# Kernel optimization log

Hardware: AMD Instinct MI355X
Metric: run time of the kernel (lower is better)

The kernel has to match this reference:

```python
import jax, jax.numpy as jnp
import numpy as np

K_SIZE = 5
PAD = 2  # (dilation*(k-1)+1 - stride + 1)//2 with k=5, dilation=1, stride=1
DEPTH_MAX = 192.0
SAMPLE_NUM = 15


def setup_inputs() -> dict:
    key = jax.random.key(0)
    k1, k2, k3, k4 = jax.random.split(key, 4)
    b, c, h, w = 2, 32, 256, 512
    depth = jax.random.uniform(k1, (b, 1, h, w), jnp.float32) * 100.0
    features = jax.random.normal(k2, (b, c, h, w), jnp.float32)
    guide_weight = jax.random.uniform(k3, (b, h, w, K_SIZE * K_SIZE), jnp.float32)
    sample_idx = jax.random.randint(k4, (SAMPLE_NUM,), 0, K_SIZE * K_SIZE, dtype=jnp.int32)
    return {"depth": depth, "features": features, "guide_weight": guide_weight,
            "sample_idx": sample_idx}


def _gather(xpad, rows, cols):
    # xpad [b,c,H+2p,W+2p]; rows [s,h], cols [s,w] -> [b,c,s,h,w]
    return xpad[:, :, rows[:, :, None], cols[:, None, :]]


def reference(depth, features, guide_weight, sample_idx):
    b, c, h, w = features.shape
    d = depth.reshape(b, h, w)
    valid = ((d > 0) & (d < DEPTH_MAX)).astype(features.dtype)[:, None]  # [b,1,h,w]

    # Gaussian positional weights of the sampled kernel offsets (select_index)
    ctr = K_SIZE // 2
    px = (sample_idx % K_SIZE).astype(jnp.float32)
    py = (sample_idx // K_SIZE).astype(jnp.float32)
    dis = jnp.sqrt((px - ctr) ** 2 + (py - ctr) ** 2)
    pos_w = jnp.exp(-0.5 * dis)
    pos_w = pos_w / jnp.sum(pos_w)  # [s]

    # Direct gather at sampled kernel offsets (equivalent to unfold + index_select).
    # torch Unfold kernel-position ordering is row-major: p -> (ky=p//K, kx=p%K).
    dy = sample_idx // K_SIZE
    dx = sample_idx % K_SIZE
    rows = dy[:, None] + jnp.arange(h)[None, :]  # [s,h] indices into padded image
    cols = dx[:, None] + jnp.arange(w)[None, :]  # [s,w]

    fpad = jnp.pad(features, ((0, 0), (0, 0), (PAD, PAD), (PAD, PAD)))
    vpad = jnp.pad(valid, ((0, 0), (0, 0), (PAD, PAD), (PAD, PAD)))

    sampled = _gather(fpad, rows, cols)            # [b,c,s,h,w]
    valid_s = _gather(vpad, rows, cols)[:, 0]      # [b,s,h,w]
    guide_s = jnp.take(guide_weight, sample_idx, axis=3)    # [b,h,w,s]
    guide_s = jnp.transpose(guide_s, (0, 3, 1, 2))          # [b,s,h,w]

    wgt = valid_s * pos_w[None, :, None, None] * guide_s    # use_position & use_guide
    wgt = jax.nn.softmax(wgt, axis=1)
    out = jnp.einsum('bcshw,bshw->bchw', sampled, wgt)
    return (out, features)
```

## Files before the change

### kernel.cpp

```cpp
#include <hip/hip_runtime.h>
#include <math.h>

#define K_SIZE 5
#define PAD 2
#define DEPTH_MAX 192.0f
#define S_NUM 15
#define G_NUM (K_SIZE * K_SIZE)

#define B_DIM 2
#define C_DIM 32
#define H_DIM 256
#define W_DIM 512
#define HW (H_DIM * W_DIM)
#define NPX (B_DIM * HW)
#define PX_PER_BLK 64
#define C_PER 8

__global__ __launch_bounds__(256) void weights_kernel(
    const float* __restrict__ depth,
    const float* __restrict__ guide,
    const int*   __restrict__ sample_idx,
    float*       __restrict__ w)
{
    __shared__ float gsh[4 * 64 * G_NUM];

    const int tid  = threadIdx.x;
    const int lane = tid & 63;
    const int wid  = tid >> 6;
    const int p    = blockIdx.x * 256 + tid;
    const int x = p % W_DIM;
    const int y = (p / W_DIM) % H_DIM;
    const int b = p / HW;

    int sidx[S_NUM];
#pragma unroll
    for (int s = 0; s < S_NUM; ++s) sidx[s] = sample_idx[s];

    {
        const int pw = blockIdx.x * 256 + (wid << 6);
        const float* gsrc = guide + (size_t)pw * G_NUM;
        float* gw = &gsh[wid * 64 * G_NUM];
#pragma unroll
        for (int k = 0; k < G_NUM; ++k)
            gw[lane + 64 * k] = gsrc[lane + 64 * k];
    }
    const float* grow = &gsh[wid * 64 * G_NUM + lane * G_NUM];

    float posw[S_NUM];
    float psum = 0.f;
#pragma unroll
    for (int s = 0; s < S_NUM; ++s) {
        const float px = (float)(sidx[s] % K_SIZE);
        const float py = (float)(sidx[s] / K_SIZE);
        const float ddx = px - (float)(K_SIZE / 2);
        const float ddy = py - (float)(K_SIZE / 2);
        posw[s] = expf(-0.5f * sqrtf(ddx * ddx + ddy * ddy));
        psum += posw[s];
    }
    const float inv_psum = 1.f / psum;

    float raw[S_NUM];
    float inb_f[S_NUM];
    const int dbase = b * HW;
#pragma unroll
    for (int s = 0; s < S_NUM; ++s) {
        const int dy = sidx[s] / K_SIZE - PAD;
        const int dx = sidx[s] % K_SIZE - PAD;
        const int yy = y + dy;
        const int xx = x + dx;
        const bool inb = (yy >= 0) & (yy < H_DIM) & (xx >= 0) & (xx < W_DIM);
        float v = 0.f;
        if (inb) {
            const float d = depth[dbase + yy * W_DIM + xx];
            v = (d > 0.f && d < DEPTH_MAX) ? 1.f : 0.f;
        }
        raw[s]   = v * (posw[s] * inv_psum) * grow[sidx[s]];
        inb_f[s] = inb ? 1.f : 0.f;
    }

    float mx = raw[0];
#pragma unroll
    for (int s = 1; s < S_NUM; ++s) mx = fmaxf(mx, raw[s]);
    float esum = 0.f;
    float wgt[S_NUM];
#pragma unroll
    for (int s = 0; s < S_NUM; ++s) {
        wgt[s] = expf(raw[s] - mx);
        esum += wgt[s];
    }
    const float inv_esum = 1.f / esum;

#pragma unroll
    for (int s = 0; s < S_NUM; ++s)
        w[s * NPX + p] = wgt[s] * inv_esum * inb_f[s];
}

__global__ __launch_bounds__(256) void gather_kernel_v2(
    const float* __restrict__ features,
    const int*   __restrict__ sample_idx,
    const float* __restrict__ w,
    float*       __restrict__ out)
{
    const int lane = threadIdx.x & 63;
    const int wid  = threadIdx.x >> 6;
    const int p = blockIdx.x * PX_PER_BLK + lane;
    const int x = p % W_DIM;
    const int y = (p / W_DIM) % H_DIM;
    const int b = p / HW;
    const int c0 = wid * C_PER;

    float wgt[S_NUM];
#pragma unroll
    for (int s = 0; s < S_NUM; ++s) wgt[s] = w[s * NPX + p];

    int sidx[S_NUM];
#pragma unroll
    for (int s = 0; s < S_NUM; ++s) sidx[s] = sample_idx[s];

    int off[S_NUM];
#pragma unroll
    for (int s = 0; s < S_NUM; ++s) {
        const int dy = sidx[s] / K_SIZE - PAD;
        const int dx = sidx[s] % K_SIZE - PAD;
        const int yy = y + dy;
        const int xx = x + dx;
        const bool inb = (yy >= 0) & (yy < H_DIM) & (xx >= 0) & (xx < W_DIM);
        off[s] = inb ? (dy * W_DIM + dx) : 0;
    }

    const size_t hw   = (size_t)HW;
    const size_t feat = (size_t)B_DIM * C_DIM * hw;
    const size_t base = ((size_t)b * C_DIM + c0) * hw + (size_t)y * W_DIM + x;
    const float* fbase = features + base;
    float*       obase = out + base;
    float*       cbase = out + feat + base;
#pragma unroll 4
    for (int c = 0; c < C_PER; ++c) {
        const float ctr = fbase[0];
        float acc = 0.f;
#pragma unroll
        for (int s = 0; s < S_NUM; ++s) {
            acc = fmaf(fbase[off[s]], wgt[s], acc);
        }
        *obase = acc;
        *cbase = ctr;
        fbase += hw;
        obase += hw;
        cbase += hw;
    }
}

__global__ __launch_bounds__(256) void adaptive_sample_fused_v3(
    const float* __restrict__ depth,
    const float* __restrict__ features,
    const float* __restrict__ guide,
    const int*   __restrict__ sample_idx,
    float*       __restrict__ out)
{
    __shared__ float gsh[PX_PER_BLK * G_NUM];
    __shared__ float wsh[PX_PER_BLK * S_NUM];

    const int lane = threadIdx.x & 63;
    const int wid  = threadIdx.x >> 6;
    const int p = blockIdx.x * PX_PER_BLK + lane;
    const int x = p % W_DIM;
    const int y = (p / W_DIM) % H_DIM;
    const int b = p / HW;
    const int c0 = wid * C_PER;

    int sidx[S_NUM];
#pragma unroll
    for (int s = 0; s < S_NUM; ++s) sidx[s] = sample_idx[s];

    if (wid == 0) {
        const float* gsrc = guide + (size_t)blockIdx.x * PX_PER_BLK * G_NUM;
#pragma unroll
        for (int k = 0; k < G_NUM; ++k)
            gsh[lane + 64 * k] = gsrc[lane + 64 * k];
        const float* grow = &gsh[lane * G_NUM];

        float posw[S_NUM];
        float psum = 0.f;
#pragma unroll
        for (int s = 0; s < S_NUM; ++s) {
            const float px = (float)(sidx[s] % K_SIZE);
            const float py = (float)(sidx[s] / K_SIZE);
            const float ddx = px - (float)(K_SIZE / 2);
            const float ddy = py - (float)(K_SIZE / 2);
            posw[s] = expf(-0.5f * sqrtf(ddx * ddx + ddy * ddy));
            psum += posw[s];
        }
        const float inv_psum = 1.f / psum;

        float raw[S_NUM];
        float inb_f[S_NUM];
        const int dbase = b * HW;
#pragma unroll
        for (int s = 0; s < S_NUM; ++s) {
            const int dy = sidx[s] / K_SIZE - PAD;
            const int dx = sidx[s] % K_SIZE - PAD;
            const int yy = y + dy;
            const int xx = x + dx;
            const bool inb = (yy >= 0) & (yy < H_DIM) & (xx >= 0) & (xx < W_DIM);
            float v = 0.f;
            if (inb) {
                const float d = depth[dbase + yy * W_DIM + xx];
                v = (d > 0.f && d < DEPTH_MAX) ? 1.f : 0.f;
            }
            raw[s]   = v * (posw[s] * inv_psum) * grow[sidx[s]];
            inb_f[s] = inb ? 1.f : 0.f;
        }

        float mx = raw[0];
#pragma unroll
        for (int s = 1; s < S_NUM; ++s) mx = fmaxf(mx, raw[s]);
        float esum = 0.f;
        float wgt[S_NUM];
#pragma unroll
        for (int s = 0; s < S_NUM; ++s) {
            wgt[s] = expf(raw[s] - mx);
            esum += wgt[s];
        }
        const float inv_esum = 1.f / esum;
#pragma unroll
        for (int s = 0; s < S_NUM; ++s)
            wsh[lane * S_NUM + s] = wgt[s] * inv_esum * inb_f[s];
    }
    __syncthreads();

    int off[S_NUM];
#pragma unroll
    for (int s = 0; s < S_NUM; ++s) {
        const int dy = sidx[s] / K_SIZE - PAD;
        const int dx = sidx[s] % K_SIZE - PAD;
        const int yy = y + dy;
        const int xx = x + dx;
        const bool inb = (yy >= 0) & (yy < H_DIM) & (xx >= 0) & (xx < W_DIM);
        off[s] = inb ? (dy * W_DIM + dx) : 0;
    }

    float wgt[S_NUM];
#pragma unroll
    for (int s = 0; s < S_NUM; ++s) wgt[s] = wsh[lane * S_NUM + s];

    const size_t hw   = (size_t)HW;
    const size_t feat = (size_t)B_DIM * C_DIM * hw;
    const size_t base = ((size_t)b * C_DIM + c0) * hw + (size_t)y * W_DIM + x;
    const float* fbase = features + base;
    float*       obase = out + base;
    float*       cbase = out + feat + base;
#pragma unroll 4
    for (int c = 0; c < C_PER; ++c) {
        const float ctr = fbase[0];
        float acc = 0.f;
#pragma unroll
        for (int s = 0; s < S_NUM; ++s) {
            acc = fmaf(fbase[off[s]], wgt[s], acc);
        }
        *obase = acc;
        *cbase = ctr;
        fbase += hw;
        obase += hw;
        cbase += hw;
    }
}

extern "C" void kernel_launch(void* const* d_in, const int* in_sizes, int n_in,
                              void* d_out, int out_size, void* d_ws, size_t ws_size,
                              hipStream_t stream) {
    const float* depth      = (const float*)d_in[0];
    const float* features   = (const float*)d_in[1];
    const float* guide      = (const float*)d_in[2];
    const int*   sample_idx = (const int*)d_in[3];

    float* out = (float*)d_out;
    const size_t ws_needed = (size_t)S_NUM * NPX * sizeof(float);
    const int blocks = NPX / PX_PER_BLK;

    if (ws_size >= ws_needed && d_ws != nullptr) {
        float* w = (float*)d_ws;
        weights_kernel<<<NPX / 256, 256, 0, stream>>>(depth, guide, sample_idx, w);
        gather_kernel_v2<<<blocks, 256, 0, stream>>>(features, sample_idx, w, out);
    } else {
        adaptive_sample_fused_v3<<<blocks, 256, 0, stream>>>(depth, features, guide,
                                                             sample_idx, out);
    }
}
```

Before: 161.1 us.

## Stage 5-row feature halo tiles in LDS with double-buffered channel loop

The gather kernel now assigns each block a 256-pixel row segment and 16 channels. It loads the 5-row stencil halo per channel into shared memory with float4 loads, double-buffering the next channel's tile while computing the current one. This replaces the 15 scattered global loads per pixel per channel with LDS reads, cutting redundant global and L2 traffic. The cost is a barrier per channel, lower grid parallelism, and clamped border loads, which rely on the precomputed zeroed weights for out-of-bounds taps.

```diff
diff --git a/kernel.cpp b/kernel.cpp
--- a/kernel.cpp
+++ b/kernel.cpp
@@ -13,8 +13,13 @@
 #define W_DIM 512
 #define HW (H_DIM * W_DIM)
 #define NPX (B_DIM * HW)
-#define PX_PER_BLK 64
-#define C_PER 8
+
+#define TX 256
+#define CH_PER 16
+#define LROW 272
+#define LDS_F (5 * LROW)
+#define NGRP (5 * 68)
+#define CTR_IDX (2 * LROW + 4)
 
 __global__ __launch_bounds__(256) void weights_kernel(
     const float* __restrict__ depth,
@@ -95,58 +100,95 @@
         w[s * NPX + p] = wgt[s] * inv_esum * inb_f[s];
 }
 
-__global__ __launch_bounds__(256) void gather_kernel_v2(
+__global__ __launch_bounds__(256) void gather_kernel_v4(
     const float* __restrict__ features,
     const int*   __restrict__ sample_idx,
     const float* __restrict__ w,
     float*       __restrict__ out)
 {
-    const int lane = threadIdx.x & 63;
-    const int wid  = threadIdx.x >> 6;
-    const int p = blockIdx.x * PX_PER_BLK + lane;
-    const int x = p % W_DIM;
-    const int y = (p / W_DIM) % H_DIM;
-    const int b = p / HW;
-    const int c0 = wid * C_PER;
-
+    __shared__ float sbuf[2][LDS_F];
+
+    const int t    = threadIdx.x;
+    const int bid  = blockIdx.x;
+    const int tile = bid & 1;
+    const int y    = (bid >> 1) & (H_DIM - 1);
+    const int b    = bid >> 9;
+    const int x0   = tile * TX;
+    const int c0   = blockIdx.y * CH_PER;
+
+    const int p = b * HW + y * W_DIM + x0 + t;
     float wgt[S_NUM];
 #pragma unroll
     for (int s = 0; s < S_NUM; ++s) wgt[s] = w[s * NPX + p];
 
-    int sidx[S_NUM];
-#pragma unroll
-    for (int s = 0; s < S_NUM; ++s) sidx[s] = sample_idx[s];
-
-    int off[S_NUM];
-#pragma unroll
-    for (int s = 0; s < S_NUM; ++s) {
-        const int dy = sidx[s] / K_SIZE - PAD;
-        const int dx = sidx[s] % K_SIZE - PAD;
-        const int yy = y + dy;
-        const int xx = x + dx;
-        const bool inb = (yy >= 0) & (yy < H_DIM) & (xx >= 0) & (xx < W_DIM);
-        off[s] = inb ? (dy * W_DIM + dx) : 0;
-    }
-
-    const size_t hw   = (size_t)HW;
+    int ldsoff[S_NUM];
+#pragma unroll
+    for (int s = 0; s < S_NUM; ++s) {
+        const int si = sample_idx[s];
+        ldsoff[s] = (si / K_SIZE) * LROW + t + (si % K_SIZE) + 2;
+    }
+
+    int lidx0, lidx1 = 0;
+    int soff0, soff1 = 0;
+    {
+        const int g   = t;
+        const int row = g / 68;
+        const int col = (g - row * 68) * 4;
+        lidx0 = row * LROW + col;
+        int ir = y + row - 2; ir = ir < 0 ? 0 : (ir > H_DIM - 1 ? H_DIM - 1 : ir);
+        int ic = x0 - 4 + col; ic = ic < 0 ? 0 : (ic > W_DIM - 4 ? W_DIM - 4 : ic);
+        soff0 = ir * W_DIM + ic;
+    }
+    const bool has2 = (t < NGRP - 256);
+    if (has2) {
+        const int g   = 256 + t;
+        const int row = g / 68;
+        const int col = (g - row * 68) * 4;
+        lidx1 = row * LROW + col;
+        int ir = y + row - 2; ir = ir < 0 ? 0 : (ir > H_DIM - 1 ? H_DIM - 1 : ir);
+        int ic = x0 - 4 + col; ic = ic < 0 ? 0 : (ic > W_DIM - 4 ? W_DIM - 4 : ic);
+        soff1 = ir * W_DIM + ic;
+    }
+
+    const size_t hw = (size_t)HW;
+    const float* fpl = features + ((size_t)b * C_DIM + c0) * hw;
     const size_t feat = (size_t)B_DIM * C_DIM * hw;
-    const size_t base = ((size_t)b * C_DIM + c0) * hw + (size_t)y * W_DIM + x;
-    const float* fbase = features + base;
-    float*       obase = out + base;
-    float*       cbase = out + feat + base;
-#pragma unroll 4
-    for (int c = 0; c < C_PER; ++c) {
-        const float ctr = fbase[0];
+    float* o0 = out + ((size_t)b * C_DIM + c0) * hw + (size_t)y * W_DIM + x0 + t;
+    float* o1 = o0 + feat;
+
+    {
+        float4 a0 = *(const float4*)(fpl + soff0);
+        float4 a1;
+        if (has2) a1 = *(const float4*)(fpl + soff1);
+        *(float4*)&sbuf[0][lidx0] = a0;
+        if (has2) *(float4*)&sbuf[0][lidx1] = a1;
+    }
+    __syncthreads();
+
+#pragma unroll
+    for (int c = 0; c < CH_PER; ++c) {
+        const int q = c & 1;
+        float4 n0, n1;
+        if (c + 1 < CH_PER) {
+            const float* fn = fpl + (size_t)(c + 1) * hw;
+            n0 = *(const float4*)(fn + soff0);
+            if (has2) n1 = *(const float4*)(fn + soff1);
+        }
+
         float acc = 0.f;
 #pragma unroll
-        for (int s = 0; s < S_NUM; ++s) {
-            acc = fmaf(fbase[off[s]], wgt[s], acc);
-        }
-        *obase = acc;
-        *cbase = ctr;
-        fbase += hw;
-        obase += hw;
-        cbase += hw;
+        for (int s = 0; s < S_NUM; ++s)
+            acc = fmaf(sbuf[q][ldsoff[s]], wgt[s], acc);
+        const float ctr = sbuf[q][CTR_IDX + t];
+
+        o0[(size_t)c * hw] = acc;
+        o1[(size_t)c * hw] = ctr;
+
+        if (c + 1 < CH_PER) {
+            *(float4*)&sbuf[q ^ 1][lidx0] = n0;
+            if (has2) *(float4*)&sbuf[q ^ 1][lidx1] = n1;
+        }
+        __syncthreads();
     }
 }
 
@@ -157,23 +199,23 @@
     const int*   __restrict__ sample_idx,
     float*       __restrict__ out)
 {
-    __shared__ float gsh[PX_PER_BLK * G_NUM];
-    __shared__ float wsh[PX_PER_BLK * S_NUM];
+    __shared__ float gsh[64 * G_NUM];
+    __shared__ float wsh[64 * S_NUM];
 
     const int lane = threadIdx.x & 63;
     const int wid  = threadIdx.x >> 6;
-    const int p = blockIdx.x * PX_PER_BLK + lane;
+    const int p = blockIdx.x * 64 + lane;
     const int x = p % W_DIM;
     const int y = (p / W_DIM) % H_DIM;
     const int b = p / HW;
-    const int c0 = wid * C_PER;
+    const int c0 = wid * 8;
 
     int sidx[S_NUM];
 #pragma unroll
     for (int s = 0; s < S_NUM; ++s) sidx[s] = sample_idx[s];
 
     if (wid == 0) {
-        const float* gsrc = guide + (size_t)blockIdx.x * PX_PER_BLK * G_NUM;
+        const float* gsrc = guide + (size_t)blockIdx.x * 64 * G_NUM;
 #pragma unroll
         for (int k = 0; k < G_NUM; ++k)
             gsh[lane + 64 * k] = gsrc[lane + 64 * k];
@@ -250,7 +292,7 @@
     float*       obase = out + base;
     float*       cbase = out + feat + base;
 #pragma unroll 4
-    for (int c = 0; c < C_PER; ++c) {
+    for (int c = 0; c < 8; ++c) {
         const float ctr = fbase[0];
         float acc = 0.f;
 #pragma unroll
@@ -275,14 +317,14 @@
 
     float* out = (float*)d_out;
     const size_t ws_needed = (size_t)S_NUM * NPX * sizeof(float);
-    const int blocks = NPX / PX_PER_BLK;
 
     if (ws_size >= ws_needed && d_ws != nullptr) {
         float* w = (float*)d_ws;
         weights_kernel<<<NPX / 256, 256, 0, stream>>>(depth, guide, sample_idx, w);
-        gather_kernel_v2<<<blocks, 256, 0, stream>>>(features, sample_idx, w, out);
+        dim3 grid(NPX / TX, C_DIM / CH_PER, 1);
+        gather_kernel_v4<<<grid, 256, 0, stream>>>(features, sample_idx, w, out);
     } else {
-        adaptive_sample_fused_v3<<<blocks, 256, 0, stream>>>(depth, features, guide,
-                                                             sample_idx, out);
+        adaptive_sample_fused_v3<<<NPX / 64, 256, 0, stream>>>(depth, features,
+                                                               guide, sample_idx, out);
     }
 }
```

New measurement: 144.8 us. -10.1%, faster.
